# Kernel optimization log

Hardware: AMD Instinct MI355X
Metric: run time of the kernel (lower is better)

## Reference

```python
import jax, jax.numpy as jnp
import numpy as np

NEG_SLOPE = 0.2  # DGL GATConv default negative_slope


def gat_conv(x, W, attn_l, attn_r, bias, src, dst, n_nodes):
    """DGL-style GATConv. x:[N,F_in], W:[F_in,H*D], attn_l/attn_r/bias:[H,D].
    Returns [N,H,D]."""
    H, D = attn_l.shape
    feat = (x @ W).reshape(n_nodes, H, D)            # projected features
    el = jnp.sum(feat * attn_l, axis=-1)              # [N,H]
    er = jnp.sum(feat * attn_r, axis=-1)              # [N,H]
    e = jax.nn.leaky_relu(el[src] + er[dst], NEG_SLOPE)  # [E,H] per-edge score
    # edge softmax over incoming edges of each dst node (numerically stable)
    m = jax.ops.segment_max(e, dst, num_segments=n_nodes)   # [N,H]
    a = jnp.exp(e - m[dst])
    denom = jax.ops.segment_sum(a, dst, num_segments=n_nodes)
    alpha = a / denom[dst]                            # [E,H]
    msg = feat[src] * alpha[..., None]                # [E,H,D]
    out = jax.ops.segment_sum(msg, dst, num_segments=n_nodes)  # [N,H,D]
    return out + bias


def setup_inputs() -> dict:
    key = jax.random.key(0)
    ks = jax.random.split(key, 12)
    N, E = 50000, 800000
    F_in, D1, H1, F_out = 128, 32, 4, 64
    h = jax.random.normal(ks[0], (N, F_in), dtype=jnp.float32)
    src = jax.random.randint(ks[1], (E,), 0, N, dtype=jnp.int32)
    dst = jax.random.randint(ks[2], (E,), 0, N, dtype=jnp.int32)
    s1 = 1.0 / np.sqrt(F_in)
    s2 = 1.0 / np.sqrt(H1 * D1)
    W1 = jax.random.normal(ks[3], (F_in, H1 * D1), dtype=jnp.float32) * s1
    al1 = jax.random.normal(ks[4], (H1, D1), dtype=jnp.float32) * s1
    ar1 = jax.random.normal(ks[5], (H1, D1), dtype=jnp.float32) * s1
    b1 = jnp.zeros((H1, D1), dtype=jnp.float32)
    W2 = jax.random.normal(ks[6], (H1 * D1, 1 * F_out), dtype=jnp.float32) * s2
    al2 = jax.random.normal(ks[7], (1, F_out), dtype=jnp.float32) * s2
    ar2 = jax.random.normal(ks[8], (1, F_out), dtype=jnp.float32) * s2
    b2 = jnp.zeros((1, F_out), dtype=jnp.float32)
    return {"h": h, "src": src, "dst": dst,
            "W1": W1, "al1": al1, "ar1": ar1, "b1": b1,
            "W2": W2, "al2": al2, "ar2": ar2, "b2": b2}


def reference(h, src, dst, W1, al1, ar1, b1, W2, al2, ar2, b2):
    N = h.shape[0]
    x = gat_conv(h, W1, al1, ar1, b1, src, dst, N)   # [N,H,D]
    x = jax.nn.relu(x.reshape(N, -1))                # flatten heads + ReLU
    # dropout(p=0.2) is identity in eval mode
    x = gat_conv(x, W2, al2, ar2, b2, src, dst, N)   # [N,1,F_out]
    return x.squeeze(1)
```

## Files before the change

### kernel.cpp

```cpp
#include <hip/hip_runtime.h>

#define NEG_SLOPE 0.2f
#define CH 4096
#define BSTRIDE 1536

__device__ inline unsigned short f2bf(float f) {
    unsigned u = __float_as_uint(f);
    unsigned r = (u + 0x7FFFu + ((u >> 16) & 1u)) >> 16;
    return (unsigned short)r;
}
__device__ inline unsigned pack2bf(float a, float b) {
    return (unsigned)f2bf(a) | ((unsigned)f2bf(b) << 16);
}
__device__ inline float bf2f_lo(unsigned u) { return __uint_as_float(u << 16); }
__device__ inline float bf2f_hi(unsigned u) { return __uint_as_float(u & 0xFFFF0000u); }
__device__ inline float lrelu(float v) { return v > 0.f ? v : NEG_SLOPE * v; }

#define FMA8(A, F, S)                          \
    A[0] = fmaf(bf2f_lo((F).x), S, A[0]);      \
    A[1] = fmaf(bf2f_hi((F).x), S, A[1]);      \
    A[2] = fmaf(bf2f_lo((F).y), S, A[2]);      \
    A[3] = fmaf(bf2f_hi((F).y), S, A[3]);      \
    A[4] = fmaf(bf2f_lo((F).z), S, A[4]);      \
    A[5] = fmaf(bf2f_hi((F).z), S, A[5]);      \
    A[6] = fmaf(bf2f_lo((F).w), S, A[6]);      \
    A[7] = fmaf(bf2f_hi((F).w), S, A[7]);

__global__ __launch_bounds__(256) void csrP_gemm1_kernel(
    const int* __restrict__ src, const int* __restrict__ dst,
    int* __restrict__ bucket_cursor, unsigned* __restrict__ tmp, int E, int NB,
    int nchunks, const float* __restrict__ h, const float* __restrict__ W1,
    const float* __restrict__ al1, const float* __restrict__ ar1,
    unsigned short* __restrict__ feat1b, float* __restrict__ el1,
    float* __restrict__ er1, int N) {
    __shared__ __align__(16) int smem[8192];
    const int tid = threadIdx.x;
    if ((int)blockIdx.x < nchunks) {
        int* lh = smem;
        int* lex = smem + 1024;
        int* gbase_sh = smem + 2048;
        int* wsum = smem + 3072;
        unsigned* sortedv = (unsigned*)(smem + 3104);
        const int base_e = blockIdx.x * CH;
        const int cnt_e = min(CH, E - base_e);
        for (int i = tid; i < 1024; i += 256) lh[i] = 0;
        __syncthreads();
        for (int i = tid; i < cnt_e; i += 256) atomicAdd(&lh[dst[base_e + i] >> 6], 1);
        __syncthreads();
        const int lane = tid & 63;
        const int wid = tid >> 6;
        int s0 = lh[tid * 4], s1 = lh[tid * 4 + 1], s2 = lh[tid * 4 + 2],
            s3 = lh[tid * 4 + 3];
        int tot = s0 + s1 + s2 + s3;
        int inc = tot;
#pragma unroll
        for (int off = 1; off < 64; off <<= 1) {
            int t = __shfl_up(inc, off, 64);
            if (lane >= off) inc += t;
        }
        if (lane == 63) wsum[wid] = inc;
        __syncthreads();
        int wbase = 0;
#pragma unroll
        for (int k = 0; k < 4; ++k)
            if (k < wid) wbase += wsum[k];
        int ebase = wbase + inc - tot;
        lex[tid * 4] = ebase;
        lex[tid * 4 + 1] = ebase + s0;
        lex[tid * 4 + 2] = ebase + s0 + s1;
        lex[tid * 4 + 3] = ebase + s0 + s1 + s2;
        for (int b = tid; b < NB; b += 256) {
            int c = lh[b];
            gbase_sh[b] = c ? atomicAdd(&bucket_cursor[b], c) : 0;
        }
        __syncthreads();
        for (int i = tid; i < 1024; i += 256) lh[i] = 0;
        __syncthreads();
        for (int i = tid; i < cnt_e; i += 256) {
            int e = base_e + i;
            int d = dst[e];
            unsigned b = (unsigned)d >> 6;
            int r = atomicAdd(&lh[b], 1);
            sortedv[lex[b] + r] =
                (b << 22) | ((unsigned)(d & 63) << 16) | (unsigned)(src[e] & 0xFFFF);
        }
        __syncthreads();
        for (int i = tid; i < cnt_e; i += 256) {
            unsigned v = sortedv[i];
            int b = v >> 22;
            int pos = gbase_sh[b] + (i - lex[b]);
            if (pos < BSTRIDE)
                tmp[(size_t)b * BSTRIDE + pos] = v;
        }
    } else {
        float* xs = (float*)smem;
        const int row0 = ((int)blockIdx.x - nchunks) * 64;
        {
            const float4* s4 = (const float4*)h;
            float4* d4 = (float4*)xs;
            int base4 = row0 * 32;
            int tot4 = N * 32;
            for (int i = tid; i < 2048; i += 256)
                if (base4 + i < tot4) d4[i] = s4[base4 + i];
        }
        __syncthreads();
        const int lane = tid & 31;
        const int c0 = lane * 4;
        const int r0 = (tid >> 5) * 8;
        float acc[8][4] = {};
#pragma unroll 2
        for (int k0 = 0; k0 < 128; k0 += 4) {
            float4 xv[8];
#pragma unroll
            for (int r = 0; r < 8; ++r)
                xv[r] = *(const float4*)(xs + (r0 + r) * 128 + k0);
#pragma unroll
            for (int kk = 0; kk < 4; ++kk) {
                float4 w = *(const float4*)(W1 + (k0 + kk) * 128 + c0);
#pragma unroll
                for (int r = 0; r < 8; ++r) {
                    float x = ((const float*)&xv[r])[kk];
                    acc[r][0] = fmaf(x, w.x, acc[r][0]);
                    acc[r][1] = fmaf(x, w.y, acc[r][1]);
                    acc[r][2] = fmaf(x, w.z, acc[r][2]);
                    acc[r][3] = fmaf(x, w.w, acc[r][3]);
                }
            }
        }
        float4 alv = *(const float4*)(al1 + c0);
        float4 arv = *(const float4*)(ar1 + c0);
#pragma unroll
        for (int r = 0; r < 8; ++r) {
            int row = row0 + r0 + r;
            if (row < N) {
                ushort4 fb;
                fb.x = f2bf(acc[r][0]);
                fb.y = f2bf(acc[r][1]);
                fb.z = f2bf(acc[r][2]);
                fb.w = f2bf(acc[r][3]);
                *(ushort4*)(feat1b + (size_t)row * 128 + c0) = fb;
                float pl = acc[r][0] * alv.x + acc[r][1] * alv.y + acc[r][2] * alv.z +
                           acc[r][3] * alv.w;
                float pr = acc[r][0] * arv.x + acc[r][1] * arv.y + acc[r][2] * arv.z +
                           acc[r][3] * arv.w;
#pragma unroll
                for (int off = 4; off >= 1; off >>= 1) {
                    pl += __shfl_xor(pl, off, 32);
                    pr += __shfl_xor(pr, off, 32);
                }
                if ((lane & 7) == 0) {
                    el1[row * 4 + (lane >> 3)] = pl;
                    er1[row * 4 + (lane >> 3)] = pr;
                }
            }
        }
    }
}

__global__ __launch_bounds__(256) void gemm2_fused(const unsigned short* __restrict__ out1b,
                                                   const float* __restrict__ W2,
                                                   const float* __restrict__ al2,
                                                   const float* __restrict__ ar2,
                                                   unsigned short* __restrict__ feat2b,
                                                   float* __restrict__ el2,
                                                   float* __restrict__ er2, int N) {
    __shared__ float xs[64 * 128];
    const int tid = threadIdx.x;
    const int row0 = blockIdx.x * 64;
    {
        const uint4* s8 = (const uint4*)out1b;
        int base8 = row0 * 16;
        int tot8 = N * 16;
        for (int i = tid; i < 1024; i += 256)
            if (base8 + i < tot8) {
                uint4 v = s8[base8 + i];
                float* o = xs + i * 8;
                o[0] = bf2f_lo(v.x);
                o[1] = bf2f_hi(v.x);
                o[2] = bf2f_lo(v.y);
                o[3] = bf2f_hi(v.y);
                o[4] = bf2f_lo(v.z);
                o[5] = bf2f_hi(v.z);
                o[6] = bf2f_lo(v.w);
                o[7] = bf2f_hi(v.w);
            }
    }
    __syncthreads();
    const int lane = tid & 15;
    const int c0 = lane * 4;
    const int r0 = (tid >> 4) * 4;
    float acc[4][4] = {};
#pragma unroll 4
    for (int k = 0; k < 128; ++k) {
        float4 w = *(const float4*)(W2 + k * 64 + c0);
#pragma unroll
        for (int r = 0; r < 4; ++r) {
            float x = xs[(r0 + r) * 128 + k];
            acc[r][0] = fmaf(x, w.x, acc[r][0]);
            acc[r][1] = fmaf(x, w.y, acc[r][1]);
            acc[r][2] = fmaf(x, w.z, acc[r][2]);
            acc[r][3] = fmaf(x, w.w, acc[r][3]);
        }
    }
    float4 alv = *(const float4*)(al2 + c0);
    float4 arv = *(const float4*)(ar2 + c0);
#pragma unroll
    for (int r = 0; r < 4; ++r) {
        int row = row0 + r0 + r;
        if (row < N) {
            ushort4 fb;
            fb.x = f2bf(acc[r][0]);
            fb.y = f2bf(acc[r][1]);
            fb.z = f2bf(acc[r][2]);
            fb.w = f2bf(acc[r][3]);
            *(ushort4*)(feat2b + (size_t)row * 64 + c0) = fb;
            float pl = acc[r][0] * alv.x + acc[r][1] * alv.y + acc[r][2] * alv.z +
                       acc[r][3] * alv.w;
            float pr = acc[r][0] * arv.x + acc[r][1] * arv.y + acc[r][2] * arv.z +
                       acc[r][3] * arv.w;
#pragma unroll
            for (int off = 8; off >= 1; off >>= 1) {
                pl += __shfl_xor(pl, off, 16);
                pr += __shfl_xor(pr, off, 16);
            }
            if (lane == 0) {
                el2[row] = pl;
                er2[row] = pr;
            }
        }
    }
}

__global__ __launch_bounds__(256) void gather1_kernel(const unsigned* __restrict__ tmp,
                                                      const int* __restrict__ bucket_cursor,
                                                      const float* __restrict__ el1,
                                                      const float* __restrict__ er1,
                                                      const unsigned short* __restrict__ feat1b,
                                                      const float* __restrict__ b1,
                                                      unsigned short* __restrict__ out1b,
                                                      int N) {
    __shared__ __align__(16) float a_all[4096];
    __shared__ int ssrc[BSTRIDE];
    __shared__ int dh[64], dex[64], dcur[64];
    unsigned* sval = (unsigned*)a_all;
    const int tid = threadIdx.x;
    const int b = (int)blockIdx.x >> 1;
    const int half = (int)blockIdx.x & 1;
    const int gb = b * BSTRIDE;
    const int cnt = min(bucket_cursor[b], BSTRIDE);
    if (tid < 64) dh[tid] = 0;
    __syncthreads();
    for (int i = tid; i < cnt; i += 256) {
        unsigned v = tmp[gb + i];
        sval[i] = v;
        atomicAdd(&dh[(v >> 16) & 63], 1);
    }
    __syncthreads();
    if (tid < 64) {
        int v = dh[tid], inc = v;
#pragma unroll
        for (int off = 1; off < 64; off <<= 1) {
            int t = __shfl_up(inc, off, 64);
            if (tid >= off) inc += t;
        }
        dex[tid] = inc - v;
        dcur[tid] = inc - v;
    }
    __syncthreads();
    for (int i = tid; i < cnt; i += 256) {
        unsigned val = sval[i];
        int dl = (val >> 16) & 63;
        int pos = atomicAdd(&dcur[dl], 1);
        ssrc[pos] = (int)((unsigned)(dl << 16) | (val & 0xFFFFu));
    }
    __syncthreads();
    const int begH = half ? dex[32] : 0;
    const int endH = half ? cnt : dex[32];
    for (int i = begH + tid; i < endH; i += 256) {
        int val = ssrc[i];
        int s = val & 0xFFFF;
        int dl = val >> 16;
        float4 el4 = *(const float4*)(el1 + (size_t)s * 4);
        float4 er4 = *(const float4*)(er1 + (size_t)(b * 64 + dl) * 4);
        float v0 = __expf(lrelu(el4.x + er4.x));
        float v1 = __expf(lrelu(el4.y + er4.y));
        float v2 = __expf(lrelu(el4.z + er4.z));
        float v3 = __expf(lrelu(el4.w + er4.w));
        int idx = i - begH;
        if (idx < 1024) *(float4*)&a_all[idx * 4] = make_float4(v0, v1, v2, v3);
    }
    __syncthreads();
    const int w = tid >> 6;
    const int lane = tid & 63;
    const int q = lane >> 4;
    const int l16 = lane & 15;
    const int c0 = l16 * 8;
    const int hh = l16 >> 2;
    float4 bv0 = *(const float4*)(b1 + c0);
    float4 bv1 = *(const float4*)(b1 + c0 + 4);
    for (int k = 0; k < 8; ++k) {
        const int dl = half * 32 + w * 8 + k;
        const int d = b * 64 + dl;
        if (d >= N) break;
        const int baseA = dex[dl];
        const int baseR = baseA - begH;
        const int M = dh[dl];
        float acc[8] = {}, bcc[8] = {};
        float den = 0.f;
        int e = q;
        for (; e + 12 < M; e += 16) {
            int s0 = ssrc[baseA + e] & 0xFFFF;
            int s1 = ssrc[baseA + e + 4] & 0xFFFF;
            int s2 = ssrc[baseA + e + 8] & 0xFFFF;
            int s3 = ssrc[baseA + e + 12] & 0xFFFF;
            float a0 = a_all[(baseR + e) * 4 + hh];
            float a1 = a_all[(baseR + e + 4) * 4 + hh];
            float a2 = a_all[(baseR + e + 8) * 4 + hh];
            float a3 = a_all[(baseR + e + 12) * 4 + hh];
            uint4 f0 = *(const uint4*)(feat1b + (size_t)s0 * 128 + c0);
            uint4 f1 = *(const uint4*)(feat1b + (size_t)s1 * 128 + c0);
            uint4 f2 = *(const uint4*)(feat1b + (size_t)s2 * 128 + c0);
            uint4 f3 = *(const uint4*)(feat1b + (size_t)s3 * 128 + c0);
            den += (a0 + a1) + (a2 + a3);
            FMA8(acc, f0, a0);
            FMA8(bcc, f1, a1);
            FMA8(acc, f2, a2);
            FMA8(bcc, f3, a3);
        }
        for (; e < M; e += 4) {
            int s0 = ssrc[baseA + e] & 0xFFFF;
            float a0 = a_all[(baseR + e) * 4 + hh];
            uint4 f0 = *(const uint4*)(feat1b + (size_t)s0 * 128 + c0);
            den += a0;
            FMA8(acc, f0, a0);
        }
#pragma unroll
        for (int j = 0; j < 8; ++j) {
            acc[j] += bcc[j];
            acc[j] += __shfl_xor(acc[j], 16, 64);
            acc[j] += __shfl_xor(acc[j], 32, 64);
        }
        den += __shfl_xor(den, 16, 64);
        den += __shfl_xor(den, 32, 64);
        if (q == 0) {
            float inv = (M > 0) ? 1.f / den : 0.f;
            uint4 o;
            o.x = pack2bf(fmaxf(acc[0] * inv + bv0.x, 0.f), fmaxf(acc[1] * inv + bv0.y, 0.f));
            o.y = pack2bf(fmaxf(acc[2] * inv + bv0.z, 0.f), fmaxf(acc[3] * inv + bv0.w, 0.f));
            o.z = pack2bf(fmaxf(acc[4] * inv + bv1.x, 0.f), fmaxf(acc[5] * inv + bv1.y, 0.f));
            o.w = pack2bf(fmaxf(acc[6] * inv + bv1.z, 0.f), fmaxf(acc[7] * inv + bv1.w, 0.f));
            *(uint4*)(out1b + (size_t)d * 128 + c0) = o;
        }
    }
}

__global__ __launch_bounds__(256) void gather2_kernel(const unsigned* __restrict__ tmp,
                                                      const int* __restrict__ bucket_cursor,
                                                      const float* __restrict__ el2,
                                                      const float* __restrict__ er2,
                                                      const unsigned short* __restrict__ feat2b,
                                                      const float* __restrict__ b2,
                                                      float* __restrict__ out2, int N) {
    __shared__ __align__(16) float a_all[BSTRIDE];
    __shared__ int ssrc[BSTRIDE];
    __shared__ int dh[64], dex[64], dcur[64];
    unsigned* sval = (unsigned*)a_all;
    const int tid = threadIdx.x;
    const int b = (int)blockIdx.x >> 1;
    const int half = (int)blockIdx.x & 1;
    const int gb = b * BSTRIDE;
    const int cnt = min(bucket_cursor[b], BSTRIDE);
    if (tid < 64) dh[tid] = 0;
    __syncthreads();
    for (int i = tid; i < cnt; i += 256) {
        unsigned v = tmp[gb + i];
        sval[i] = v;
        atomicAdd(&dh[(v >> 16) & 63], 1);
    }
    __syncthreads();
    if (tid < 64) {
        int v = dh[tid], inc = v;
#pragma unroll
        for (int off = 1; off < 64; off <<= 1) {
            int t = __shfl_up(inc, off, 64);
            if (tid >= off) inc += t;
        }
        dex[tid] = inc - v;
        dcur[tid] = inc - v;
    }
    __syncthreads();
    for (int i = tid; i < cnt; i += 256) {
        unsigned val = sval[i];
        int dl = (val >> 16) & 63;
        int pos = atomicAdd(&dcur[dl], 1);
        ssrc[pos] = (int)((unsigned)(dl << 16) | (val & 0xFFFFu));
    }
    __syncthreads();
    const int begH = half ? dex[32] : 0;
    const int endH = half ? cnt : dex[32];
    for (int i = begH + tid; i < endH; i += 256) {
        int val = ssrc[i];
        int s = val & 0xFFFF;
        int dl = val >> 16;
        float v = el2[s] + er2[b * 64 + dl];
        a_all[i] = __expf(lrelu(v));
    }
    __syncthreads();
    const int w = tid >> 6;
    const int lane = tid & 63;
    const int oct = lane >> 3;
    const int l8 = lane & 7;
    const int c0 = l8 * 8;
    float4 bv0 = *(const float4*)(b2 + c0);
    float4 bv1 = *(const float4*)(b2 + c0 + 4);
    for (int k = 0; k < 8; ++k) {
        const int dl = half * 32 + w * 8 + k;
        const int d = b * 64 + dl;
        if (d >= N) break;
        const int base = dex[dl];
        const int M = dh[dl];
        float acc[8] = {}, bcc[8] = {};
        float den = 0.f;
        int e = oct;
        for (; e + 8 < M; e += 16) {
            int s0 = ssrc[base + e] & 0xFFFF;
            int s1 = ssrc[base + e + 8] & 0xFFFF;
            float a0 = a_all[base + e];
            float a1 = a_all[base + e + 8];
            uint4 f0 = *(const uint4*)(feat2b + (size_t)s0 * 64 + c0);
            uint4 f1 = *(const uint4*)(feat2b + (size_t)s1 * 64 + c0);
            den += a0 + a1;
            FMA8(acc, f0, a0);
            FMA8(bcc, f1, a1);
        }
        while (e < M) {
            int s0 = ssrc[base + e] & 0xFFFF;
            float a0 = a_all[base + e];
            uint4 f0 = *(const uint4*)(feat2b + (size_t)s0 * 64 + c0);
            den += a0;
            FMA8(acc, f0, a0);
            e += 8;
        }
#pragma unroll
        for (int j = 0; j < 8; ++j) {
            acc[j] += bcc[j];
            acc[j] += __shfl_xor(acc[j], 8, 64);
            acc[j] += __shfl_xor(acc[j], 16, 64);
            acc[j] += __shfl_xor(acc[j], 32, 64);
        }
        den += __shfl_xor(den, 8, 64);
        den += __shfl_xor(den, 16, 64);
        den += __shfl_xor(den, 32, 64);
        if (oct == 0) {
            float inv = (M > 0) ? 1.f / den : 0.f;
            *(float4*)(out2 + (size_t)d * 64 + c0) =
                make_float4(acc[0] * inv + bv0.x, acc[1] * inv + bv0.y,
                            acc[2] * inv + bv0.z, acc[3] * inv + bv0.w);
            *(float4*)(out2 + (size_t)d * 64 + c0 + 4) =
                make_float4(acc[4] * inv + bv1.x, acc[5] * inv + bv1.y,
                            acc[6] * inv + bv1.z, acc[7] * inv + bv1.w);
        }
    }
}

extern "C" void kernel_launch(void* const* d_in, const int* in_sizes, int n_in,
                              void* d_out, int out_size, void* d_ws, size_t ws_size,
                              hipStream_t stream) {
    const float* h   = (const float*)d_in[0];
    const int*   src = (const int*)d_in[1];
    const int*   dst = (const int*)d_in[2];
    const float* W1  = (const float*)d_in[3];
    const float* al1 = (const float*)d_in[4];
    const float* ar1 = (const float*)d_in[5];
    const float* b1  = (const float*)d_in[6];
    const float* W2  = (const float*)d_in[7];
    const float* al2 = (const float*)d_in[8];
    const float* ar2 = (const float*)d_in[9];
    const float* b2  = (const float*)d_in[10];

    const int N = in_sizes[0] / 128;
    const int E = in_sizes[1];
    const int NB = (N + 63) >> 6;

    char* ws = (char*)d_ws;
    size_t off = 0;
    auto alloc = [&](size_t elems) -> void* {
        void* p = (void*)(ws + off);
        off += ((elems * 4 + 255) / 256) * 256;
        return p;
    };
    int* bucket_cursor = (int*)alloc(NB);
    unsigned* tmp      = (unsigned*)alloc((size_t)NB * BSTRIDE);
    float* el1   = (float*)alloc((size_t)N * 4);
    float* er1   = (float*)alloc((size_t)N * 4);
    unsigned short* feat1b = (unsigned short*)alloc((size_t)N * 64);
    unsigned short* out1b  = (unsigned short*)alloc((size_t)N * 64);
    float* el2   = (float*)alloc(N);
    float* er2   = (float*)alloc(N);
    unsigned short* feat2b = (unsigned short*)alloc((size_t)N * 32);
    float* out2  = (float*)d_out;

    const int nchunks = (E + CH - 1) / CH;
    const int gemm1_blocks = (N + 63) / 64;

    hipMemsetAsync(bucket_cursor, 0, (size_t)NB * 4, stream);
    csrP_gemm1_kernel<<<nchunks + gemm1_blocks, 256, 0, stream>>>(
        src, dst, bucket_cursor, tmp, E, NB, nchunks, h, W1, al1, ar1, feat1b,
        el1, er1, N);

    gather1_kernel<<<NB * 2, 256, 0, stream>>>(tmp, bucket_cursor, el1, er1,
                                               feat1b, b1, out1b, N);

    gemm2_fused<<<(N + 63) / 64, 256, 0, stream>>>(out1b, W2, al2, ar2, feat2b, el2,
                                                   er2, N);
    gather2_kernel<<<NB * 2, 256, 0, stream>>>(tmp, bucket_cursor, el2, er2,
                                               feat2b, b2, out2, N);
}
```

Before: 216.5 us.

## Hoist weight loads in GEMM loops and double gather block size

Both GEMM inner loops now load their weight vectors before the FMA chain, batching four or eight rows of W per step, so global loads are issued up front instead of interleaved with the arithmetic. The gather kernels move from 256 to 512 threads per block, so each wave handles four destination nodes instead of eight and the staging loops use twice as many threads. The aim is more parallelism per bucket and better latency hiding, at the cost of more registers in the GEMMs and larger blocks that may lower how many blocks fit per CU.

```diff
diff --git a/kernel.cpp b/kernel.cpp
--- a/kernel.cpp
+++ b/kernel.cpp
@@ -110,21 +110,32 @@
         float acc[8][4] = {};
 #pragma unroll 2
         for (int k0 = 0; k0 < 128; k0 += 4) {
+            float4 wv0 = *(const float4*)(W1 + (k0 + 0) * 128 + c0);
+            float4 wv1 = *(const float4*)(W1 + (k0 + 1) * 128 + c0);
+            float4 wv2 = *(const float4*)(W1 + (k0 + 2) * 128 + c0);
+            float4 wv3 = *(const float4*)(W1 + (k0 + 3) * 128 + c0);
             float4 xv[8];
 #pragma unroll
             for (int r = 0; r < 8; ++r)
                 xv[r] = *(const float4*)(xs + (r0 + r) * 128 + k0);
 #pragma unroll
-            for (int kk = 0; kk < 4; ++kk) {
-                float4 w = *(const float4*)(W1 + (k0 + kk) * 128 + c0);
-#pragma unroll
-                for (int r = 0; r < 8; ++r) {
-                    float x = ((const float*)&xv[r])[kk];
-                    acc[r][0] = fmaf(x, w.x, acc[r][0]);
-                    acc[r][1] = fmaf(x, w.y, acc[r][1]);
-                    acc[r][2] = fmaf(x, w.z, acc[r][2]);
-                    acc[r][3] = fmaf(x, w.w, acc[r][3]);
-                }
+            for (int r = 0; r < 8; ++r) {
+                acc[r][0] = fmaf(xv[r].x, wv0.x, acc[r][0]);
+                acc[r][1] = fmaf(xv[r].x, wv0.y, acc[r][1]);
+                acc[r][2] = fmaf(xv[r].x, wv0.z, acc[r][2]);
+                acc[r][3] = fmaf(xv[r].x, wv0.w, acc[r][3]);
+                acc[r][0] = fmaf(xv[r].y, wv1.x, acc[r][0]);
+                acc[r][1] = fmaf(xv[r].y, wv1.y, acc[r][1]);
+                acc[r][2] = fmaf(xv[r].y, wv1.z, acc[r][2]);
+                acc[r][3] = fmaf(xv[r].y, wv1.w, acc[r][3]);
+                acc[r][0] = fmaf(xv[r].z, wv2.x, acc[r][0]);
+                acc[r][1] = fmaf(xv[r].z, wv2.y, acc[r][1]);
+                acc[r][2] = fmaf(xv[r].z, wv2.z, acc[r][2]);
+                acc[r][3] = fmaf(xv[r].z, wv2.w, acc[r][3]);
+                acc[r][0] = fmaf(xv[r].w, wv3.x, acc[r][0]);
+                acc[r][1] = fmaf(xv[r].w, wv3.y, acc[r][1]);
+                acc[r][2] = fmaf(xv[r].w, wv3.z, acc[r][2]);
+                acc[r][3] = fmaf(xv[r].w, wv3.w, acc[r][3]);
             }
         }
         float4 alv = *(const float4*)(al1 + c0);
@@ -190,16 +201,21 @@
     const int c0 = lane * 4;
     const int r0 = (tid >> 4) * 4;
     float acc[4][4] = {};
-#pragma unroll 4
-    for (int k = 0; k < 128; ++k) {
-        float4 w = *(const float4*)(W2 + k * 64 + c0);
-#pragma unroll
-        for (int r = 0; r < 4; ++r) {
-            float x = xs[(r0 + r) * 128 + k];
-            acc[r][0] = fmaf(x, w.x, acc[r][0]);
-            acc[r][1] = fmaf(x, w.y, acc[r][1]);
-            acc[r][2] = fmaf(x, w.z, acc[r][2]);
-            acc[r][3] = fmaf(x, w.w, acc[r][3]);
+    for (int k0 = 0; k0 < 128; k0 += 8) {
+        float4 wv[8];
+#pragma unroll
+        for (int kk = 0; kk < 8; ++kk)
+            wv[kk] = *(const float4*)(W2 + (k0 + kk) * 64 + c0);
+#pragma unroll
+        for (int kk = 0; kk < 8; ++kk) {
+#pragma unroll
+            for (int r = 0; r < 4; ++r) {
+                float x = xs[(r0 + r) * 128 + k0 + kk];
+                acc[r][0] = fmaf(x, wv[kk].x, acc[r][0]);
+                acc[r][1] = fmaf(x, wv[kk].y, acc[r][1]);
+                acc[r][2] = fmaf(x, wv[kk].z, acc[r][2]);
+                acc[r][3] = fmaf(x, wv[kk].w, acc[r][3]);
+            }
         }
     }
     float4 alv = *(const float4*)(al2 + c0);
@@ -231,7 +247,7 @@
     }
 }
 
-__global__ __launch_bounds__(256) void gather1_kernel(const unsigned* __restrict__ tmp,
+__global__ __launch_bounds__(512) void gather1_kernel(const unsigned* __restrict__ tmp,
                                                       const int* __restrict__ bucket_cursor,
                                                       const float* __restrict__ el1,
                                                       const float* __restrict__ er1,
@@ -250,7 +266,7 @@
     const int cnt = min(bucket_cursor[b], BSTRIDE);
     if (tid < 64) dh[tid] = 0;
     __syncthreads();
-    for (int i = tid; i < cnt; i += 256) {
+    for (int i = tid; i < cnt; i += 512) {
         unsigned v = tmp[gb + i];
         sval[i] = v;
         atomicAdd(&dh[(v >> 16) & 63], 1);
@@ -267,7 +283,7 @@
         dcur[tid] = inc - v;
     }
     __syncthreads();
-    for (int i = tid; i < cnt; i += 256) {
+    for (int i = tid; i < cnt; i += 512) {
         unsigned val = sval[i];
         int dl = (val >> 16) & 63;
         int pos = atomicAdd(&dcur[dl], 1);
@@ -276,7 +292,7 @@
     __syncthreads();
     const int begH = half ? dex[32] : 0;
     const int endH = half ? cnt : dex[32];
-    for (int i = begH + tid; i < endH; i += 256) {
+    for (int i = begH + tid; i < endH; i += 512) {
         int val = ssrc[i];
         int s = val & 0xFFFF;
         int dl = val >> 16;
@@ -298,8 +314,8 @@
     const int hh = l16 >> 2;
     float4 bv0 = *(const float4*)(b1 + c0);
     float4 bv1 = *(const float4*)(b1 + c0 + 4);
-    for (int k = 0; k < 8; ++k) {
-        const int dl = half * 32 + w * 8 + k;
+    for (int k = 0; k < 4; ++k) {
+        const int dl = half * 32 + w * 4 + k;
         const int d = b * 64 + dl;
         if (d >= N) break;
         const int baseA = dex[dl];
@@ -354,7 +370,7 @@
     }
 }
 
-__global__ __launch_bounds__(256) void gather2_kernel(const unsigned* __restrict__ tmp,
+__global__ __launch_bounds__(512) void gather2_kernel(const unsigned* __restrict__ tmp,
                                                       const int* __restrict__ bucket_cursor,
                                                       const float* __restrict__ el2,
                                                       const float* __restrict__ er2,
@@ -372,7 +388,7 @@
     const int cnt = min(bucket_cursor[b], BSTRIDE);
     if (tid < 64) dh[tid] = 0;
     __syncthreads();
-    for (int i = tid; i < cnt; i += 256) {
+    for (int i = tid; i < cnt; i += 512) {
         unsigned v = tmp[gb + i];
         sval[i] = v;
         atomicAdd(&dh[(v >> 16) & 63], 1);
@@ -389,7 +405,7 @@
         dcur[tid] = inc - v;
     }
     __syncthreads();
-    for (int i = tid; i < cnt; i += 256) {
+    for (int i = tid; i < cnt; i += 512) {
         unsigned val = sval[i];
         int dl = (val >> 16) & 63;
         int pos = atomicAdd(&dcur[dl], 1);
@@ -398,7 +414,7 @@
     __syncthreads();
     const int begH = half ? dex[32] : 0;
     const int endH = half ? cnt : dex[32];
-    for (int i = begH + tid; i < endH; i += 256) {
+    for (int i = begH + tid; i < endH; i += 512) {
         int val = ssrc[i];
         int s = val & 0xFFFF;
         int dl = val >> 16;
@@ -413,8 +429,8 @@
     const int c0 = l8 * 8;
     float4 bv0 = *(const float4*)(b2 + c0);
     float4 bv1 = *(const float4*)(b2 + c0 + 4);
-    for (int k = 0; k < 8; ++k) {
-        const int dl = half * 32 + w * 8 + k;
+    for (int k = 0; k < 4; ++k) {
+        const int dl = half * 32 + w * 4 + k;
         const int d = b * 64 + dl;
         if (d >= N) break;
         const int base = dex[dl];
@@ -508,11 +524,11 @@
         src, dst, bucket_cursor, tmp, E, NB, nchunks, h, W1, al1, ar1, feat1b,
         el1, er1, N);
 
-    gather1_kernel<<<NB * 2, 256, 0, stream>>>(tmp, bucket_cursor, el1, er1,
+    gather1_kernel<<<NB * 2, 512, 0, stream>>>(tmp, bucket_cursor, el1, er1,
                                                feat1b, b1, out1b, N);
 
     gemm2_fused<<<(N + 63) / 64, 256, 0, stream>>>(out1b, W2, al2, ar2, feat2b, el2,
                                                    er2, N);
-    gather2_kernel<<<NB * 2, 256, 0, stream>>>(tmp, bucket_cursor, el2, er2,
+    gather2_kernel<<<NB * 2, 512, 0, stream>>>(tmp, bucket_cursor, el2, er2,
                                                feat2b, b2, out2, N);
 }
```

New measurement: 209.7 us. -3.2%, faster.
